# Kernel optimization log

Measured on AMD Instinct MI355X. Metric: run time of the kernel, lower is better.

The kernel has to match this reference:

```python
import jax, jax.numpy as jnp
import numpy as np

B, D = 8192, 1024
TEMPERATURE = 0.5


def _normalize(x, eps=1e-12):
    # matches torch F.normalize(dim=-1): x / max(||x||, eps)
    n = jnp.sqrt(jnp.sum(x * x, axis=-1, keepdims=True))
    return x / jnp.maximum(n, eps)


def setup_inputs() -> dict:
    key = jax.random.key(0)
    k1, k2 = jax.random.split(key)
    z_i = jax.random.normal(k1, (B, D), dtype=jnp.float32)
    z_j = jax.random.normal(k2, (B, D), dtype=jnp.float32)
    return {"z_i": z_i, "z_j": z_j}


def reference(z_i, z_j):
    b = z_i.shape[0]
    zi = _normalize(z_i)
    zj = _normalize(z_j)
    # cross-block cosine similarities: logits[:B, B:] == zi @ zj.T
    sim = jnp.einsum('id,jd->ij', zi, zj) / TEMPERATURE  # [B, B]
    labels = jnp.arange(b)
    # cross_entropy with integer targets: mean of -log_softmax[i, labels[i]]
    lsm_i = jax.nn.log_softmax(sim, axis=-1)      # rows: image -> text
    lsm_j = jax.nn.log_softmax(sim.T, axis=-1)    # rows: text -> image
    loss_i = -jnp.mean(lsm_i[labels, labels])
    loss_j = -jnp.mean(lsm_j[labels, labels])
    return (loss_i + loss_j) * 0.5
```

## Files before the change

kernel.cpp:

```cpp
#include <hip/hip_runtime.h>
#include <hip/hip_bf16.h>


using f32x4 = __attribute__((ext_vector_type(4))) float;
using i32x8 = __attribute__((ext_vector_type(8))) int;
using i32x4 = __attribute__((ext_vector_type(4))) int;

#define USCL 0x7F7F7F7Fu

__device__ __forceinline__ void async16(const unsigned char* g, unsigned char* l) {
    __builtin_amdgcn_global_load_lds(
        (const __attribute__((address_space(1))) void*)g,
        (__attribute__((address_space(3))) void*)l, 16, 0, 0);
}

__global__ __launch_bounds__(256) void clip_norm_k(const float* __restrict__ in,
                                                   unsigned int* __restrict__ out,
                                                   float extra) {
    int row = blockIdx.x;
    const float4* ip = reinterpret_cast<const float4*>(in + (size_t)row * 1024);
    float4 v = ip[threadIdx.x];
    float ss = v.x * v.x + v.y * v.y + v.z * v.z + v.w * v.w;
    #pragma unroll
    for (int o = 1; o < 64; o <<= 1) ss += __shfl_xor(ss, o);
    __shared__ float sb[4];
    if ((threadIdx.x & 63) == 0) sb[threadIdx.x >> 6] = ss;
    __syncthreads();
    float tot = sb[0] + sb[1] + sb[2] + sb[3];
    float scl = extra / fmaxf(sqrtf(tot), 1e-12f);
    int p = __builtin_amdgcn_cvt_pk_fp8_f32(v.x * scl, v.y * scl, 0, false);
    p = __builtin_amdgcn_cvt_pk_fp8_f32(v.z * scl, v.w * scl, p, true);
    out[(size_t)row * 256 + threadIdx.x] = (unsigned int)p;
}

__device__ __forceinline__ i32x8 ldfrag(const unsigned char* buf, int row, int khi) {
    int p0 = (2 * khi) ^ (row & 7);
    int p1 = (2 * khi + 1) ^ (row & 7);
    i32x4 lo = *reinterpret_cast<const i32x4*>(buf + row * 128 + p0 * 16);
    i32x4 hi = *reinterpret_cast<const i32x4*>(buf + row * 128 + p1 * 16);
    i32x8 r;
    r[0] = lo[0]; r[1] = lo[1]; r[2] = lo[2]; r[3] = lo[3];
    r[4] = hi[0]; r[5] = hi[1]; r[6] = hi[2]; r[7] = hi[3];
    return r;
}

__global__ __launch_bounds__(256, 2) void clip_gemm_k(
    const unsigned char* __restrict__ A,
    const unsigned char* __restrict__ Bm,
    float* __restrict__ rp, float* __restrict__ cp, float* __restrict__ dg) {
    __shared__ unsigned char bA0[16384], bB0[16384], bA1[16384], bB1[16384];
    __shared__ float rbuf[2][128];
    __shared__ float cbuf[2][128];

    const int c_x = blockIdx.x & 7;
    const int q = blockIdx.x >> 3;
    const int s = q >> 6;
    const int p = q & 63;
    const int bi = c_x * 8 + (p >> 3);
    const int bj = s * 8 + (p & 7);
    const int tid = threadIdx.x;
    const int l = tid & 63, w = tid >> 6;
    const int wm = w >> 1, wn = w & 1;
    const int llo = l & 15, khi = l >> 4;

    f32x4 acc[4][4] = {};

    const unsigned char* Ag = A + (size_t)(bi * 128) * 1024;
    const unsigned char* Bg = Bm + (size_t)(bj * 128) * 1024;

    int soff[4];
    #pragma unroll
    for (int u = 0; u < 4; ++u) {
        int idx = u * 256 + tid;
        int srow = idx >> 3;
        int clog = idx & 7;
        soff[u] = srow * 1024 + ((clog ^ (srow & 7)) * 16);
    }
    const int ldst = tid * 16;

#define STAGE(ktB, bufA, bufB)                                            \
    _Pragma("unroll") for (int u = 0; u < 4; ++u)                         \
        async16(Ag + (ktB) + soff[u], (bufA) + u * 4096 + ldst);          \
    _Pragma("unroll") for (int u = 0; u < 4; ++u)                         \
        async16(Bg + (ktB) + soff[u], (bufB) + u * 4096 + ldst);

    STAGE(0, bA0, bB0)
    asm volatile("s_waitcnt vmcnt(0)" ::: "memory");
    __builtin_amdgcn_s_barrier();
    __builtin_amdgcn_sched_barrier(0);

    for (int t = 0; t < 8; ++t) {
        const unsigned char* Ac = (t & 1) ? bA1 : bA0;
        const unsigned char* Bc = (t & 1) ? bB1 : bB0;
        unsigned char* Asg = (t & 1) ? bA0 : bA1;
        unsigned char* Bsg = (t & 1) ? bB0 : bB1;

        if (t <= 6) { STAGE((t + 1) * 128, Asg, Bsg) }

        i32x8 af[4], bfr[4];
        #pragma unroll
        for (int m = 0; m < 4; ++m)
            af[m] = ldfrag(Ac, wm * 64 + m * 16 + llo, khi);
        #pragma unroll
        for (int n = 0; n < 4; ++n)
            bfr[n] = ldfrag(Bc, wn * 64 + n * 16 + llo, khi);
        #pragma unroll
        for (int m = 0; m < 4; ++m)
            #pragma unroll
            for (int n = 0; n < 4; ++n)
                acc[m][n] = __builtin_amdgcn_mfma_scale_f32_16x16x128_f8f6f4(
                    af[m], bfr[n], acc[m][n], 0, 0, 0, USCL, 0, USCL);

        if (t <= 6) {
            asm volatile("s_waitcnt vmcnt(0) lgkmcnt(0)" ::: "memory");
            __builtin_amdgcn_s_barrier();
            __builtin_amdgcn_sched_barrier(0);
        }
    }
#undef STAGE

    if (bi == bj && wm == wn) {
        #pragma unroll
        for (int m = 0; m < 4; ++m)
            #pragma unroll
            for (int r = 0; r < 4; ++r)
                if (khi * 4 + r == llo)
                    dg[bi * 128 + wm * 64 + m * 16 + llo] = acc[m][m][r];
    }

    #pragma unroll
    for (int m = 0; m < 4; ++m)
        #pragma unroll
        for (int n = 0; n < 4; ++n)
            #pragma unroll
            for (int r = 0; r < 4; ++r)
                acc[m][n][r] = exp2f(acc[m][n][r] * 1.44269504f);

    #pragma unroll
    for (int m = 0; m < 4; ++m) {
        #pragma unroll
        for (int r = 0; r < 4; ++r) {
            float v = acc[m][0][r] + acc[m][1][r] + acc[m][2][r] + acc[m][3][r];
            v += __shfl_xor(v, 1);
            v += __shfl_xor(v, 2);
            v += __shfl_xor(v, 4);
            v += __shfl_xor(v, 8);
            if (llo == 0) rbuf[wn][wm * 64 + m * 16 + khi * 4 + r] = v;
        }
    }
    #pragma unroll
    for (int n = 0; n < 4; ++n) {
        float v = 0.f;
        #pragma unroll
        for (int m = 0; m < 4; ++m)
            v += acc[m][n][0] + acc[m][n][1] + acc[m][n][2] + acc[m][n][3];
        v += __shfl_xor(v, 16);
        v += __shfl_xor(v, 32);
        if (khi == 0) cbuf[wm][wn * 64 + n * 16 + llo] = v;
    }
    __syncthreads();
    if (tid < 128) {
        rp[(size_t)bj * 8192 + bi * 128 + tid] = rbuf[0][tid] + rbuf[1][tid];
        cp[(size_t)bi * 8192 + bj * 128 + tid] = cbuf[0][tid] + cbuf[1][tid];
    }
}

__global__ __launch_bounds__(256) void clip_fin1_k(const float* __restrict__ rp,
                                                   const float* __restrict__ cp,
                                                   const float* __restrict__ dg,
                                                   float* __restrict__ part) {
    int i = blockIdx.x * 256 + threadIdx.x;
    float rs = 0.f, cs = 0.f;
    #pragma unroll 8
    for (int b = 0; b < 64; ++b) rs += rp[(size_t)b * 8192 + i];
    #pragma unroll 8
    for (int b = 0; b < 64; ++b) cs += cp[(size_t)b * 8192 + i];
    float c = 0.5f * (logf(rs) + logf(cs)) - dg[i];
    #pragma unroll
    for (int o = 1; o < 64; o <<= 1) c += __shfl_xor(c, o);
    __shared__ float sb[4];
    if ((threadIdx.x & 63) == 0) sb[threadIdx.x >> 6] = c;
    __syncthreads();
    if (threadIdx.x == 0) part[blockIdx.x] = sb[0] + sb[1] + sb[2] + sb[3];
}

__global__ void clip_fin2_k(const float* __restrict__ part, float* __restrict__ out) {
    float v = (threadIdx.x < 32) ? part[threadIdx.x] : 0.f;
    #pragma unroll
    for (int o = 1; o < 64; o <<= 1) v += __shfl_xor(v, o);
    if (threadIdx.x == 0) out[0] = v * (1.f / 8192.f);
}

extern "C" void kernel_launch(void* const* d_in, const int* in_sizes, int n_in,
                              void* d_out, int out_size, void* d_ws, size_t ws_size,
                              hipStream_t stream) {
    const float* zi = (const float*)d_in[0];
    const float* zj = (const float*)d_in[1];
    float* out = (float*)d_out;
    char* ws = (char*)d_ws;

    unsigned int* zi8 = (unsigned int*)(ws);
    unsigned int* zj8 = (unsigned int*)(ws + (size_t)8 * 1024 * 1024);
    float* rp   = (float*)(ws + (size_t)16 * 1024 * 1024);
    float* cp   = (float*)(ws + (size_t)18 * 1024 * 1024);
    float* dg   = (float*)(ws + (size_t)20 * 1024 * 1024);
    float* part = (float*)(ws + (size_t)20 * 1024 * 1024 + 32768);

    clip_norm_k<<<8192, 256, 0, stream>>>(zi, zi8, 2.0f);
    clip_norm_k<<<8192, 256, 0, stream>>>(zj, zj8, 1.0f);
    clip_gemm_k<<<4096, 256, 0, stream>>>((const unsigned char*)zi8,
                                          (const unsigned char*)zj8, rp, cp, dg);
    clip_fin1_k<<<32, 256, 0, stream>>>(rp, cp, dg, part);
    clip_fin2_k<<<1, 64, 0, stream>>>(part, out);
}
```

Measured before the change: 125.7 us.

## Load B fragments directly from global memory instead of staging through LDS

Drops the LDS double buffers for the B operand in the fp8 GEMM. Each wave now reads its B MFMA fragments straight from global memory (two 16-byte loads per fragment) while A is still staged asynchronously through LDS. This halves LDS use per block, which may allow more resident blocks, and removes the LDS write and read traffic for B. In exchange, both waves that share a wn column fetch the same B data from global memory or L2, and these loads sit on the critical path right before the MFMAs with no prefetch.

```diff
diff --git a/kernel.cpp b/kernel.cpp
--- a/kernel.cpp
+++ b/kernel.cpp
@@ -44,11 +44,22 @@
     return r;
 }
 
+__device__ __forceinline__ i32x8 ldBg(const unsigned char* Bg, int row, int khi,
+                                      int ktB) {
+    const unsigned char* p = Bg + (size_t)row * 1024 + ktB + khi * 32;
+    i32x4 lo = *reinterpret_cast<const i32x4*>(p);
+    i32x4 hi = *reinterpret_cast<const i32x4*>(p + 16);
+    i32x8 r;
+    r[0] = lo[0]; r[1] = lo[1]; r[2] = lo[2]; r[3] = lo[3];
+    r[4] = hi[0]; r[5] = hi[1]; r[6] = hi[2]; r[7] = hi[3];
+    return r;
+}
+
 __global__ __launch_bounds__(256, 2) void clip_gemm_k(
     const unsigned char* __restrict__ A,
     const unsigned char* __restrict__ Bm,
     float* __restrict__ rp, float* __restrict__ cp, float* __restrict__ dg) {
-    __shared__ unsigned char bA0[16384], bB0[16384], bA1[16384], bB1[16384];
+    __shared__ unsigned char bA0[16384], bA1[16384];
     __shared__ float rbuf[2][128];
     __shared__ float cbuf[2][128];
 
@@ -78,32 +89,29 @@
     }
     const int ldst = tid * 16;
 
-#define STAGE(ktB, bufA, bufB)                                            \
+#define STAGE_A(ktB, bufA)                                                \
     _Pragma("unroll") for (int u = 0; u < 4; ++u)                         \
-        async16(Ag + (ktB) + soff[u], (bufA) + u * 4096 + ldst);          \
-    _Pragma("unroll") for (int u = 0; u < 4; ++u)                         \
-        async16(Bg + (ktB) + soff[u], (bufB) + u * 4096 + ldst);
-
-    STAGE(0, bA0, bB0)
+        async16(Ag + (ktB) + soff[u], (bufA) + u * 4096 + ldst);
+
+    STAGE_A(0, bA0)
     asm volatile("s_waitcnt vmcnt(0)" ::: "memory");
     __builtin_amdgcn_s_barrier();
     __builtin_amdgcn_sched_barrier(0);
 
     for (int t = 0; t < 8; ++t) {
         const unsigned char* Ac = (t & 1) ? bA1 : bA0;
-        const unsigned char* Bc = (t & 1) ? bB1 : bB0;
         unsigned char* Asg = (t & 1) ? bA0 : bA1;
-        unsigned char* Bsg = (t & 1) ? bB0 : bB1;
-
-        if (t <= 6) { STAGE((t + 1) * 128, Asg, Bsg) }
-
-        i32x8 af[4], bfr[4];
+
+        if (t <= 6) { STAGE_A((t + 1) * 128, Asg) }
+
+        i32x8 bfr[4];
+        #pragma unroll
+        for (int n = 0; n < 4; ++n)
+            bfr[n] = ldBg(Bg, wn * 64 + n * 16 + llo, khi, t * 128);
+        i32x8 af[4];
         #pragma unroll
         for (int m = 0; m < 4; ++m)
             af[m] = ldfrag(Ac, wm * 64 + m * 16 + llo, khi);
-        #pragma unroll
-        for (int n = 0; n < 4; ++n)
-            bfr[n] = ldfrag(Bc, wn * 64 + n * 16 + llo, khi);
         #pragma unroll
         for (int m = 0; m < 4; ++m)
             #pragma unroll
@@ -117,7 +125,7 @@
             __builtin_amdgcn_sched_barrier(0);
         }
     }
-#undef STAGE
+#undef STAGE_A
 
     if (bi == bj && wm == wn) {
         #pragma unroll
```

Result: slower. 194.0 us (+54.3%).

## Load GEMM fragments directly from global memory instead of LDS staging

Applied to the files above, without the earlier changes.

Removes the double-buffered async global-to-LDS staging, the barriers and the swizzled LDS fragment reads. Each wave now loads its MFMA operand fragments straight from global memory through the caches. This drops LDS traffic and synchronisation. In exchange, operands shared between waves are fetched redundantly, and the explicit prefetch overlap is gone.

```diff
diff --git a/kernel.cpp b/kernel.cpp
--- a/kernel.cpp
+++ b/kernel.cpp
@@ -7,12 +7,6 @@
 using i32x4 = __attribute__((ext_vector_type(4))) int;
 
 #define USCL 0x7F7F7F7Fu
-
-__device__ __forceinline__ void async16(const unsigned char* g, unsigned char* l) {
-    __builtin_amdgcn_global_load_lds(
-        (const __attribute__((address_space(1))) void*)g,
-        (__attribute__((address_space(3))) void*)l, 16, 0, 0);
-}
 
 __global__ __launch_bounds__(256) void clip_norm_k(const float* __restrict__ in,
                                                    unsigned int* __restrict__ out,
@@ -33,11 +27,11 @@
     out[(size_t)row * 256 + threadIdx.x] = (unsigned int)p;
 }
 
-__device__ __forceinline__ i32x8 ldfrag(const unsigned char* buf, int row, int khi) {
-    int p0 = (2 * khi) ^ (row & 7);
-    int p1 = (2 * khi + 1) ^ (row & 7);
-    i32x4 lo = *reinterpret_cast<const i32x4*>(buf + row * 128 + p0 * 16);
-    i32x4 hi = *reinterpret_cast<const i32x4*>(buf + row * 128 + p1 * 16);
+__device__ __forceinline__ i32x8 ldG(const unsigned char* G, int row, int khi,
+                                     int ktB) {
+    const unsigned char* p = G + (size_t)row * 1024 + ktB + khi * 32;
+    i32x4 lo = *reinterpret_cast<const i32x4*>(p);
+    i32x4 hi = *reinterpret_cast<const i32x4*>(p + 16);
     i32x8 r;
     r[0] = lo[0]; r[1] = lo[1]; r[2] = lo[2]; r[3] = lo[3];
     r[4] = hi[0]; r[5] = hi[1]; r[6] = hi[2]; r[7] = hi[3];
@@ -48,7 +42,6 @@
     const unsigned char* __restrict__ A,
     const unsigned char* __restrict__ Bm,
     float* __restrict__ rp, float* __restrict__ cp, float* __restrict__ dg) {
-    __shared__ unsigned char bA0[16384], bB0[16384], bA1[16384], bB1[16384];
     __shared__ float rbuf[2][128];
     __shared__ float cbuf[2][128];
 
@@ -68,56 +61,22 @@
     const unsigned char* Ag = A + (size_t)(bi * 128) * 1024;
     const unsigned char* Bg = Bm + (size_t)(bj * 128) * 1024;
 
-    int soff[4];
     #pragma unroll
-    for (int u = 0; u < 4; ++u) {
-        int idx = u * 256 + tid;
-        int srow = idx >> 3;
-        int clog = idx & 7;
-        soff[u] = srow * 1024 + ((clog ^ (srow & 7)) * 16);
-    }
-    const int ldst = tid * 16;
-
-#define STAGE(ktB, bufA, bufB)                                            \
-    _Pragma("unroll") for (int u = 0; u < 4; ++u)                         \
-        async16(Ag + (ktB) + soff[u], (bufA) + u * 4096 + ldst);          \
-    _Pragma("unroll") for (int u = 0; u < 4; ++u)                         \
-        async16(Bg + (ktB) + soff[u], (bufB) + u * 4096 + ldst);
-
-    STAGE(0, bA0, bB0)
-    asm volatile("s_waitcnt vmcnt(0)" ::: "memory");
-    __builtin_amdgcn_s_barrier();
-    __builtin_amdgcn_sched_barrier(0);
-
     for (int t = 0; t < 8; ++t) {
-        const unsigned char* Ac = (t & 1) ? bA1 : bA0;
-        const unsigned char* Bc = (t & 1) ? bB1 : bB0;
-        unsigned char* Asg = (t & 1) ? bA0 : bA1;
-        unsigned char* Bsg = (t & 1) ? bB0 : bB1;
-
-        if (t <= 6) { STAGE((t + 1) * 128, Asg, Bsg) }
-
         i32x8 af[4], bfr[4];
         #pragma unroll
         for (int m = 0; m < 4; ++m)
-            af[m] = ldfrag(Ac, wm * 64 + m * 16 + llo, khi);
+            af[m] = ldG(Ag, wm * 64 + m * 16 + llo, khi, t * 128);
         #pragma unroll
         for (int n = 0; n < 4; ++n)
-            bfr[n] = ldfrag(Bc, wn * 64 + n * 16 + llo, khi);
+            bfr[n] = ldG(Bg, wn * 64 + n * 16 + llo, khi, t * 128);
         #pragma unroll
         for (int m = 0; m < 4; ++m)
             #pragma unroll
             for (int n = 0; n < 4; ++n)
                 acc[m][n] = __builtin_amdgcn_mfma_scale_f32_16x16x128_f8f6f4(
                     af[m], bfr[n], acc[m][n], 0, 0, 0, USCL, 0, USCL);
-
-        if (t <= 6) {
-            asm volatile("s_waitcnt vmcnt(0) lgkmcnt(0)" ::: "memory");
-            __builtin_amdgcn_s_barrier();
-            __builtin_amdgcn_sched_barrier(0);
-        }
     }
-#undef STAGE
 
     if (bi == bj && wm == wn) {
         #pragma unroll
```

Result: slower. 271.1 us (+115.7%).
